# Kernel optimization log

Measured on AMD Instinct MI355X. Metric: run time of the kernel, lower is better.

## Reference

```python
import jax, jax.numpy as jnp
import numpy as np

NCAPS, NHIDDEN, NLAYER, ROUTIT = 8, 16, 2, 6
CUT = 5


def _normalize(v, axis):
    return v / jnp.maximum(jnp.linalg.norm(v, axis=axis, keepdims=True), 1e-12)


def _routing(x, nb_flat, k, max_iter, last):
    # x: [n, d] flat features, nb_flat: [n*m] neighbor ids (-1 = pad)
    n, d = x.shape
    dd = d // k
    m = nb_flat.shape[0] // n
    x3 = _normalize(x.reshape(n, k, dd), axis=2)              # [n,k,dd]
    x_c = jnp.concatenate([x3.reshape(n, d), jnp.zeros((1, d), x.dtype)], 0)  # [n+1,d]
    nbm = jnp.where(nb_flat < 0, n, nb_flat)
    z = x_c[nbm].reshape(n, m, k, dd)                         # neighbor gather
    u = None
    p = None
    for it in range(max_iter):
        p = jnp.zeros((n, m, k), x.dtype) if u is None else jnp.einsum('nmkc,nkc->nmk', z, u)
        p = jax.nn.softmax(p, axis=2)
        u = jnp.einsum('nmkc,nmk->nkc', z, p) + x3
        if it < max_iter - 1:
            u = _normalize(u, axis=2)
    if not last:
        return u.reshape(n, d)
    # meta-path aggregation (last layer)
    nb2 = nb_flat.reshape(n, m)
    nei_mask = (nb2 >= 0).astype(x.dtype)
    p1 = jnp.argmax(p, axis=2)                                # [n,m]
    A = jax.nn.one_hot(p1, k, dtype=x.dtype) * nei_mask[:, :, None]  # [n,m,k]
    Ai = A.transpose(2, 0, 1).astype(jnp.int32)               # [k,n,m]
    B = Ai * nb2[None].astype(jnp.int32) + (Ai - 1)           # nb where assigned, else -1
    B = jnp.concatenate([B, -jnp.ones((k, 1, m), jnp.int32)], axis=1)  # [k,n+1,m]
    mapB = jnp.where(B < 0, n, B)                             # -1 -> zero row n
    sel = mapB[:, :, :CUT]                                    # [k,n+1,CUT]
    x_c3 = x_c.reshape(n + 1, k, dd)
    gather_j = jax.vmap(lambda idx, xj: xj[idx], in_axes=(0, 1))  # over capsule j
    metas = []
    for i in range(k):
        # two-hop neighbors through capsule i then capsule j
        tmp = mapB[:, sel[i].reshape(-1), :CUT].reshape(k, n + 1, CUT * CUT)[:, :n]  # [k,n,25]
        hj = gather_j(tmp, x_c3)                               # [k,n,25,dd]
        metas.append(hj.mean(axis=2))                          # [k,n,dd]
    meta = jnp.stack(metas, 0)                                 # [i,j,n,dd]
    meta = meta.sum(axis=1).transpose(1, 0, 2)                 # sum over j -> [n,k,dd]
    meta = u + meta
    return u.reshape(n, d), meta.reshape(n, d)


def setup_inputs() -> dict:
    key = jax.random.key(0)
    ks = jax.random.split(key, 10)
    n, nfeat, nclass = 20000, 500, 16
    m = 32
    d = NCAPS * NHIDDEN
    return {
        'x': jax.random.normal(ks[0], (n, nfeat), jnp.float32),
        'nb': jax.random.randint(ks[1], (n, m), 0, n, jnp.int64),
        'pca_w': jax.random.normal(ks[2], (nfeat, d), jnp.float32) * 0.05,
        'pca_b': jax.random.normal(ks[3], (d,), jnp.float32) * 0.05,
        'ln_g': jnp.ones((NHIDDEN,), jnp.float32),
        'ln_b': jnp.zeros((NHIDDEN,), jnp.float32),
        'w_qs': jax.random.normal(ks[4], (NHIDDEN, NHIDDEN), jnp.float32) * 0.1,
        'w_ks': jax.random.normal(ks[5], (NHIDDEN, NHIDDEN), jnp.float32) * 0.1,
        'mlp_w': jax.random.normal(ks[6], (d, nclass), jnp.float32) * 0.05,
        'mlp_b': jax.random.normal(ks[7], (nclass,), jnp.float32) * 0.05,
    }


def reference(x, nb, pca_w, pca_b, ln_g, ln_b, w_qs, w_ks, mlp_w, mlp_b):
    k, dd = NCAPS, NHIDDEN
    n = x.shape[0]
    nb_flat = nb.reshape(-1)
    h = x @ pca_w + pca_b                                      # [n, d]
    h3 = h.reshape(n, k, dd)
    # Independence attention over capsules (only attn matters; output q is discarded)
    mu = h3.mean(-1, keepdims=True)
    var = ((h3 - mu) ** 2).mean(-1, keepdims=True)
    q = (h3 - mu) / jnp.sqrt(var + 1e-6) * ln_g + ln_b
    q = q @ w_qs                                               # [n,k,dd]
    kk = h3 @ w_ks
    temp = jnp.asarray(dd, x.dtype) ** 0.5
    attn = jax.nn.softmax(jnp.einsum('nqc,nkc->nqk', q / temp, kk), axis=-1)  # [n,k,k]
    off = 1.0 - jnp.eye(k, dtype=x.dtype)
    attn_loss = (attn * off).sum() / (off.sum() * n)
    h = jax.nn.relu(h3).reshape(n, k * dd)
    meta = None
    for layer in range(NLAYER):
        last = layer == NLAYER - 1
        if last:
            u, meta = _routing(h, nb_flat, k, ROUTIT, True)
        else:
            h = jax.nn.relu(_routing(h, nb_flat, k, ROUTIT, False))
    meta = jax.nn.relu(meta) @ mlp_w + mlp_b
    return jax.nn.log_softmax(meta, axis=1), attn_loss, meta
```

## Files before the change

kernel.cpp:

```cpp
#include <hip/hip_runtime.h>
#include <math.h>

#define NCAPS 8
#define DD    16
#define D     128
#define M     32
#define ROUTIT 6
#define CUT   5

__device__ __forceinline__ float wred16_sum(float v) {
    v += __shfl_xor(v, 1);
    v += __shfl_xor(v, 2);
    v += __shfl_xor(v, 4);
    v += __shfl_xor(v, 8);
    return v;
}

typedef _Float16 h2 __attribute__((ext_vector_type(2)));
union U32H2 { unsigned u; h2 h; };
__device__ __forceinline__ unsigned pack_h2(float a, float b) {
    U32H2 r; r.h.x = (_Float16)a; r.h.y = (_Float16)b; return r.u;
}
__device__ __forceinline__ h2 ash2(unsigned u) { U32H2 r; r.u = u; return r.h; }

__global__ void init_kernel(float* xc0, float* xc1, int n) {
    int t = threadIdx.x;
    if (t < D) {
        xc0[(size_t)n * D + t] = 0.f;
        xc1[(size_t)n * D + t] = 0.f;
    }
}

__global__ __launch_bounds__(256) void pca_attn(
        const float* __restrict__ x, const float* __restrict__ w,
        const float* __restrict__ bias, const float* __restrict__ ln_g,
        const float* __restrict__ ln_b, const float* __restrict__ w_qs,
        const float* __restrict__ w_ks, float* __restrict__ xc0,
        float* __restrict__ partial, int n, int nfeat) {
    __shared__ float xs[20][36];
    __shared__ alignas(16) float ws[20][128];
    __shared__ alignas(16) float hs[32][132];
    __shared__ alignas(16) float ks[32][8][20];
    __shared__ float wq[256], wk[256];
    __shared__ float red[4];
    const int tid = threadIdx.x;
    const int cg = tid & 31;
    const int rg = tid >> 5;
    const int row0 = blockIdx.x * 32;
    wq[tid] = w_qs[tid];
    wk[tid] = w_ks[tid];
    const float4 bi4 = *(const float4*)&bias[cg * 4];

    float acc[4][4] = {};
    for (int k0 = 0; k0 < nfeat; k0 += 20) {
        if (tid < 160) {
            int r = tid / 5, cf = tid % 5;
            int row = row0 + r;
            float4 f = (row < n)
                ? *(const float4*)&x[(size_t)row * nfeat + k0 + cf * 4]
                : make_float4(0.f, 0.f, 0.f, 0.f);
            xs[cf * 4 + 0][r] = f.x; xs[cf * 4 + 1][r] = f.y;
            xs[cf * 4 + 2][r] = f.z; xs[cf * 4 + 3][r] = f.w;
        }
#pragma unroll
        for (int i = 0; i < 3; ++i) {
            int f = tid + i * 256;
            if (f < 640) {
                int kk = f >> 5, c4 = f & 31;
                *(float4*)&ws[kk][c4 * 4] =
                    *(const float4*)&w[(size_t)(k0 + kk) * 128 + c4 * 4];
            }
        }
        __syncthreads();
#pragma unroll
        for (int kk = 0; kk < 20; ++kk) {
            float4 a = *(const float4*)&xs[kk][rg * 4];
            float4 b = *(const float4*)&ws[kk][cg * 4];
            float av[4] = {a.x, a.y, a.z, a.w};
            float bv[4] = {b.x, b.y, b.z, b.w};
#pragma unroll
            for (int i = 0; i < 4; ++i)
#pragma unroll
                for (int j = 0; j < 4; ++j) acc[i][j] += av[i] * bv[j];
        }
        __syncthreads();
    }
#pragma unroll
    for (int i = 0; i < 4; ++i)
        *(float4*)&hs[rg * 4 + i][cg * 4] =
            make_float4(acc[i][0] + bi4.x, acc[i][1] + bi4.y,
                        acc[i][2] + bi4.z, acc[i][3] + bi4.w);
    __syncthreads();

    const int r = tid >> 3, kq = tid & 7;
    const int row = row0 + r;
    float hv[16], q[16], kk[16];
    if (row < n) {
#pragma unroll
        for (int i = 0; i < 4; ++i) {
            float4 f = *(const float4*)&hs[r][kq * 16 + i * 4];
            hv[i * 4 + 0] = f.x; hv[i * 4 + 1] = f.y;
            hv[i * 4 + 2] = f.z; hv[i * 4 + 3] = f.w;
        }
        float mu = 0.f;
#pragma unroll
        for (int c = 0; c < 16; ++c) mu += hv[c];
        mu *= (1.f / 16.f);
        float var = 0.f;
#pragma unroll
        for (int c = 0; c < 16; ++c) { float d = hv[c] - mu; var += d * d; }
        var *= (1.f / 16.f);
        float rstd = rsqrtf(var + 1e-6f);
        float qn[16];
#pragma unroll
        for (int c = 0; c < 16; ++c)
            qn[c] = (hv[c] - mu) * rstd * ln_g[c] + ln_b[c];
#pragma unroll
        for (int c = 0; c < 16; ++c) { q[c] = 0.f; kk[c] = 0.f; }
#pragma unroll
        for (int cp = 0; cp < 16; ++cp)
#pragma unroll
            for (int c = 0; c < 16; ++c) {
                q[c]  += qn[cp] * wq[cp * 16 + c];
                kk[c] += hv[cp] * wk[cp * 16 + c];
            }
#pragma unroll
        for (int c = 0; c < 16; ++c) q[c] *= 0.25f;
#pragma unroll
        for (int i = 0; i < 4; ++i)
            *(float4*)&ks[r][kq][i * 4] =
                make_float4(kk[i * 4], kk[i * 4 + 1], kk[i * 4 + 2], kk[i * 4 + 3]);
        float ss = 0.f;
        float rl[16];
#pragma unroll
        for (int c = 0; c < 16; ++c) { rl[c] = fmaxf(hv[c], 0.f); ss += rl[c] * rl[c]; }
        float inv = 1.f / fmaxf(sqrtf(ss), 1e-12f);
        float4* xo = (float4*)(xc0 + (size_t)row * D + kq * DD);
#pragma unroll
        for (int i = 0; i < 4; ++i)
            xo[i] = make_float4(rl[i * 4] * inv, rl[i * 4 + 1] * inv,
                                rl[i * 4 + 2] * inv, rl[i * 4 + 3] * inv);
    }
    __syncthreads();

    float offd = 0.f;
    if (row < n) {
        float s[8];
#pragma unroll
        for (int j = 0; j < 8; ++j) {
            float d = 0.f;
#pragma unroll
            for (int i = 0; i < 4; ++i) {
                float4 f = *(const float4*)&ks[r][j][i * 4];
                d += q[i * 4] * f.x + q[i * 4 + 1] * f.y
                   + q[i * 4 + 2] * f.z + q[i * 4 + 3] * f.w;
            }
            s[j] = d;
        }
        float mx = s[0];
#pragma unroll
        for (int j = 1; j < 8; ++j) mx = fmaxf(mx, s[j]);
        float e[8], se = 0.f;
#pragma unroll
        for (int j = 0; j < 8; ++j) { e[j] = __expf(s[j] - mx); se += e[j]; }
        float rse = 1.f / se;
#pragma unroll
        for (int j = 0; j < 8; ++j)
            if (j != kq) offd += e[j] * rse;
    }
    offd += __shfl_xor(offd, 1);
    offd += __shfl_xor(offd, 2);
    offd += __shfl_xor(offd, 4);
    offd += __shfl_xor(offd, 8);
    offd += __shfl_xor(offd, 16);
    offd += __shfl_xor(offd, 32);
    int lane = tid & 63, wid = tid >> 6;
    if (lane == 0) red[wid] = offd;
    __syncthreads();
    if (tid == 0) partial[blockIdx.x] = red[0] + red[1] + red[2] + red[3];
}

__global__ __launch_bounds__(256) void reduce_kernel(
        const float* __restrict__ partial, float* __restrict__ acc, int npart) {
    __shared__ float red[4];
    const int t = threadIdx.x;
    float s = 0.f;
    for (int i = t; i < npart; i += 256) s += partial[i];
    s += __shfl_xor(s, 1);  s += __shfl_xor(s, 2);
    s += __shfl_xor(s, 4);  s += __shfl_xor(s, 8);
    s += __shfl_xor(s, 16); s += __shfl_xor(s, 32);
    if ((t & 63) == 0) red[t >> 6] = s;
    __syncthreads();
    if (t == 0) acc[0] = red[0] + red[1] + red[2] + red[3];
}

template <bool LAST>
__global__ __launch_bounds__(64) void routing_kernel(
        const float* __restrict__ xc,
        const int* __restrict__ nb,
        float* __restrict__ out,
        int* __restrict__ amax, int n) {
    __shared__ alignas(16) uint2 zsu[M * 32];
    __shared__ alignas(8)  uint2 usu[NCAPS * 5];
    __shared__ alignas(16) float pT[NCAPS * 36];
    const int l = threadIdx.x;
    const int v = blockIdx.x;
    const int m  = l & 31;
    const int kh = l >> 5;
    const int f4 = m;
    const int mg = kh;

    {
        int sm = l >> 1, sh = l & 1;
        int src = 0;
        if (l < M) {
            int nbv = nb[(size_t)v * M + l];
            src = (nbv < 0) ? n : nbv;
        }
        int srow = __shfl(src, sm);
        const float4* g = (const float4*)(xc + (size_t)srow * D);
#pragma unroll
        for (int i = 0; i < 16; ++i) {
            int f = sh * 16 + i;
            float4 zf = g[f];
            zsu[sm * 32 + (f ^ sm)] =
                make_uint2(pack_h2(zf.x, zf.y), pack_h2(zf.z, zf.w));
        }
    }
    float4 x3 = ((const float4*)(xc + (size_t)v * D))[f4];
    __syncthreads();

    {
        float4 a = make_float4(0.f, 0.f, 0.f, 0.f);
#pragma unroll
        for (int j = 0; j < 16; ++j) {
            int r = mg * 16 + j;
            uint2 zz = zsu[r * 32 + (f4 ^ r)];
            h2 lo = ash2(zz.x), hi = ash2(zz.y);
            a.x += (float)lo.x; a.y += (float)lo.y;
            a.z += (float)hi.x; a.w += (float)hi.y;
        }
        a.x += __shfl_xor(a.x, 32); a.y += __shfl_xor(a.y, 32);
        a.z += __shfl_xor(a.z, 32); a.w += __shfl_xor(a.w, 32);
        a.x = a.x * 0.125f + x3.x;  a.y = a.y * 0.125f + x3.y;
        a.z = a.z * 0.125f + x3.z;  a.w = a.w * 0.125f + x3.w;
        float ss = a.x * a.x + a.y * a.y + a.z * a.z + a.w * a.w;
        ss += __shfl_xor(ss, 1); ss += __shfl_xor(ss, 2);
        float inv = 1.f / fmaxf(sqrtf(ss), 1e-12f);
        if (l < 32)
            usu[(f4 >> 2) * 5 + (f4 & 3)] =
                make_uint2(pack_h2(a.x * inv, a.y * inv),
                           pack_h2(a.z * inv, a.w * inv));
    }
    __syncthreads();

    for (int it = 1; it < ROUTIT; ++it) {
        float pr[4];
#pragma unroll
        for (int j = 0; j < 4; ++j) {
            float s = 0.f;
            const uint2* uk = &usu[(kh * 4 + j) * 5];
#pragma unroll
            for (int c2 = 0; c2 < 4; ++c2) {
                int f = kh * 16 + j * 4 + c2;
                uint2 zz = zsu[m * 32 + (f ^ m)];
                uint2 uu = uk[c2];
                s = __builtin_amdgcn_fdot2(ash2(zz.x), ash2(uu.x), s, false);
                s = __builtin_amdgcn_fdot2(ash2(zz.y), ash2(uu.y), s, false);
            }
            pr[j] = s;
        }
        float po[4];
#pragma unroll
        for (int j = 0; j < 4; ++j) po[j] = __shfl_xor(pr[j], 32);
        if (LAST && it == ROUTIT - 1) {
            float p8[8];
#pragma unroll
            for (int j = 0; j < 4; ++j) {
                p8[kh * 4 + j] = pr[j];
                p8[(kh ^ 1) * 4 + j] = po[j];
            }
            float bv = p8[0]; int bi = 0;
#pragma unroll
            for (int k2 = 1; k2 < 8; ++k2)
                if (p8[k2] > bv) { bv = p8[k2]; bi = k2; }
            if (l < 32) amax[(size_t)v * M + m] = bi;
        }
        float er[4], S = 0.f;
#pragma unroll
        for (int j = 0; j < 4; ++j) { er[j] = __expf(pr[j]); S += er[j]; }
#pragma unroll
        for (int j = 0; j < 4; ++j) S += __expf(po[j]);
        float rS = 1.f / S;
#pragma unroll
        for (int j = 0; j < 4; ++j)
            pT[(kh * 4 + j) * 36 + m] = er[j] * rS;
        __syncthreads();

        float pk[16];
        {
            const int k2 = f4 >> 2;
#pragma unroll
            for (int j4 = 0; j4 < 4; ++j4) {
                float4 pp = *(const float4*)&pT[k2 * 36 + mg * 16 + j4 * 4];
                pk[j4 * 4 + 0] = pp.x; pk[j4 * 4 + 1] = pp.y;
                pk[j4 * 4 + 2] = pp.z; pk[j4 * 4 + 3] = pp.w;
            }
        }
        float4 a = make_float4(0.f, 0.f, 0.f, 0.f);
#pragma unroll
        for (int j = 0; j < 16; ++j) {
            int r = mg * 16 + j;
            uint2 zz = zsu[r * 32 + (f4 ^ r)];
            h2 lo = ash2(zz.x), hi = ash2(zz.y);
            a.x += (float)lo.x * pk[j]; a.y += (float)lo.y * pk[j];
            a.z += (float)hi.x * pk[j]; a.w += (float)hi.y * pk[j];
        }
        a.x += __shfl_xor(a.x, 32); a.y += __shfl_xor(a.y, 32);
        a.z += __shfl_xor(a.z, 32); a.w += __shfl_xor(a.w, 32);
        a.x += x3.x; a.y += x3.y; a.z += x3.z; a.w += x3.w;

        if (it < ROUTIT - 1) {
            float ss = a.x * a.x + a.y * a.y + a.z * a.z + a.w * a.w;
            ss += __shfl_xor(ss, 1); ss += __shfl_xor(ss, 2);
            float inv = 1.f / fmaxf(sqrtf(ss), 1e-12f);
            if (l < 32)
                usu[(f4 >> 2) * 5 + (f4 & 3)] =
                    make_uint2(pack_h2(a.x * inv, a.y * inv),
                               pack_h2(a.z * inv, a.w * inv));
            __syncthreads();
        } else if (LAST) {
            if (l < 32) ((float4*)(out + (size_t)v * D))[f4] = a;
        } else {
            float r0 = fmaxf(a.x, 0.f), r1 = fmaxf(a.y, 0.f);
            float r2 = fmaxf(a.z, 0.f), r3 = fmaxf(a.w, 0.f);
            float ss = r0 * r0 + r1 * r1 + r2 * r2 + r3 * r3;
            ss += __shfl_xor(ss, 1); ss += __shfl_xor(ss, 2);
            float inv = 1.f / fmaxf(sqrtf(ss), 1e-12f);
            if (l < 32)
                ((float4*)(out + (size_t)v * D))[f4] =
                    make_float4(r0 * inv, r1 * inv, r2 * inv, r3 * inv);
        }
    }
}

__global__ __launch_bounds__(256) void s2_kernel(
        const float* __restrict__ xc1, const int* __restrict__ nb,
        const int* __restrict__ amax, float* __restrict__ s2, int n) {
    int idx = blockIdx.x * 256 + threadIdx.x;
    if (idx >= n * 16) return;
    int w = idx >> 4, c = idx & 15;
    float s = 0.f;
#pragma unroll
    for (int b = 0; b < CUT; ++b) {
        int t  = nb[(size_t)w * M + b];
        int jj = amax[(size_t)w * M + b];
        int im = (t < 0) ? n : t;
        s += xc1[(size_t)im * D + jj * DD + c];
    }
    s2[idx] = s;
}

__global__ __launch_bounds__(256) void meta_kernel(
        const float* __restrict__ u1, const float* __restrict__ s2,
        const int* __restrict__ nb, const int* __restrict__ amax,
        const float* __restrict__ mlp_w, const float* __restrict__ mlp_b,
        const float* __restrict__ attn_acc, float* __restrict__ d_out, int n) {
    __shared__ float Wl[128 * 16];
    __shared__ float accs[16][132];
    const int t = threadIdx.x;
#pragma unroll
    for (int i = 0; i < 8; ++i) Wl[t + i * 256] = mlp_w[t + i * 256];
    const int g = t >> 4, c = t & 15;
    const int v = blockIdx.x * 16 + g;
    if (blockIdx.x == 0 && t == 0)
        d_out[(size_t)n * 16] = attn_acc[0] * (1.f / (56.f * (float)n));
    if (v < n) {
#pragma unroll
        for (int i = 0; i < 8; ++i) accs[g][i * 16 + c] = 0.f;
        for (int a = 0; a < CUT; ++a) {
            int w = nb[(size_t)v * M + a];
            if (w < 0) continue;
            int i = amax[(size_t)v * M + a];
            accs[g][i * 16 + c] += s2[(size_t)w * 16 + c];
        }
#pragma unroll
        for (int i = 0; i < 8; ++i) {
            float meta = u1[(size_t)v * D + i * 16 + c] + accs[g][i * 16 + c] * (1.f / 25.f);
            accs[g][i * 16 + c] = fmaxf(meta, 0.f);
        }
    }
    __syncthreads();
    if (v < n) {
        float o = mlp_b[c];
#pragma unroll
        for (int dd = 0; dd < 128; ++dd) o += accs[g][dd] * Wl[dd * 16 + c];
        float mx = o;
        mx = fmaxf(mx, __shfl_xor(mx, 1));
        mx = fmaxf(mx, __shfl_xor(mx, 2));
        mx = fmaxf(mx, __shfl_xor(mx, 4));
        mx = fmaxf(mx, __shfl_xor(mx, 8));
        float e = __expf(o - mx);
        float se = wred16_sum(e);
        float ls = (o - mx) - logf(se);
        d_out[(size_t)v * 16 + c] = ls;
        d_out[(size_t)n * 16 + 1 + (size_t)v * 16 + c] = o;
    }
}

extern "C" void kernel_launch(void* const* d_in, const int* in_sizes, int n_in,
                              void* d_out, int out_size, void* d_ws, size_t ws_size,
                              hipStream_t stream) {
    const float* x     = (const float*)d_in[0];
    const int*   nb    = (const int*)d_in[1];
    const float* pca_w = (const float*)d_in[2];
    const float* pca_b = (const float*)d_in[3];
    const float* ln_g  = (const float*)d_in[4];
    const float* ln_b  = (const float*)d_in[5];
    const float* w_qs  = (const float*)d_in[6];
    const float* w_ks  = (const float*)d_in[7];
    const float* mlp_w = (const float*)d_in[8];
    const float* mlp_b = (const float*)d_in[9];
    float* out = (float*)d_out;

    const int d = 128;
    const int nfeat = in_sizes[2] / d;
    const int n = in_sizes[0] / nfeat;
    const int nblk = (n + 31) / 32;

    float* bufA = (float*)d_ws;
    float* bufB = bufA + (size_t)n * d;
    float* bufC = bufB + (size_t)(n + 1) * d;
    float* acc  = bufC + (size_t)(n + 1) * d;
    int* amax = (int*)bufB;
    float* s2 = bufB + (size_t)n * M;
    float* partial = bufC;

    init_kernel<<<1, 256, 0, stream>>>(bufB, bufC, n);
    pca_attn<<<nblk, 256, 0, stream>>>(x, pca_w, pca_b, ln_g, ln_b, w_qs, w_ks,
                                       bufB, partial, n, nfeat);
    reduce_kernel<<<1, 256, 0, stream>>>(partial, acc, nblk);
    routing_kernel<false><<<n, 64, 0, stream>>>(bufB, nb, bufC, nullptr, n);
    routing_kernel<true><<<n, 64, 0, stream>>>(bufC, nb, bufA, amax, n);
    s2_kernel<<<(n * 16 + 255) / 256, 256, 0, stream>>>(bufC, nb, amax, s2, n);
    meta_kernel<<<(n + 15) / 16, 256, 0, stream>>>(bufA, s2, nb, amax, mlp_w, mlp_b, acc, out, n);
}
```

Measured before the change: 286.6 us.

## Use fp16 packed dot2 and register prefetch in PCA matmul

The PCA projection GEMM now converts input and weight tiles to packed fp16 pairs in shared memory and accumulates with v_dot2 (fdot2) in fp32. The next tile's global loads are prefetched into registers during the current tile's compute, so one barrier per tile is removed. Shared buffers are aliased to save LDS. This trades input precision (fp16 rounding of x and W) for fewer FMAs and less LDS traffic, which adds some accuracy risk.

```diff
diff --git a/kernel.cpp b/kernel.cpp
--- a/kernel.cpp
+++ b/kernel.cpp
@@ -37,10 +37,11 @@
         const float* __restrict__ ln_b, const float* __restrict__ w_qs,
         const float* __restrict__ w_ks, float* __restrict__ xc0,
         float* __restrict__ partial, int n, int nfeat) {
-    __shared__ float xs[20][36];
-    __shared__ alignas(16) float ws[20][128];
+    __shared__ alignas(16) unsigned char uS[20480];
+    unsigned (*xs2)[36]  = (unsigned(*)[36])uS;
+    unsigned (*ws2)[128] = (unsigned(*)[128])(uS + 1440);
+    float (*ks)[8][20]   = (float(*)[8][20])uS;
     __shared__ alignas(16) float hs[32][132];
-    __shared__ alignas(16) float ks[32][8][20];
     __shared__ float wq[256], wk[256];
     __shared__ float red[4];
     const int tid = threadIdx.x;
@@ -51,39 +52,75 @@
     wk[tid] = w_ks[tid];
     const float4 bi4 = *(const float4*)&bias[cg * 4];
 
+    const int xr_r = tid / 5, xr_cf = tid % 5;
+    const int wk0 = tid >> 5, wc0 = tid & 31;
+    float4 xr{}, w0a{}, w0b{}, w1a{}, w1b{};
+
+    {
+        if (tid < 160) {
+            int row = row0 + xr_r;
+            xr = (row < n) ? *(const float4*)&x[(size_t)row * nfeat + xr_cf * 4]
+                           : make_float4(0.f, 0.f, 0.f, 0.f);
+        }
+        w0a = *(const float4*)&w[(size_t)(2 * wk0) * 128 + wc0 * 4];
+        w0b = *(const float4*)&w[(size_t)(2 * wk0 + 1) * 128 + wc0 * 4];
+        if (tid < 64) {
+            int kkp = 8 + (tid >> 5);
+            w1a = *(const float4*)&w[(size_t)(2 * kkp) * 128 + wc0 * 4];
+            w1b = *(const float4*)&w[(size_t)(2 * kkp + 1) * 128 + wc0 * 4];
+        }
+    }
     float acc[4][4] = {};
-    for (int k0 = 0; k0 < nfeat; k0 += 20) {
+    const int ntile = nfeat / 20;
+    for (int t = 0; t < ntile; ++t) {
+        __syncthreads();
         if (tid < 160) {
-            int r = tid / 5, cf = tid % 5;
-            int row = row0 + r;
-            float4 f = (row < n)
-                ? *(const float4*)&x[(size_t)row * nfeat + k0 + cf * 4]
-                : make_float4(0.f, 0.f, 0.f, 0.f);
-            xs[cf * 4 + 0][r] = f.x; xs[cf * 4 + 1][r] = f.y;
-            xs[cf * 4 + 2][r] = f.z; xs[cf * 4 + 3][r] = f.w;
-        }
-#pragma unroll
-        for (int i = 0; i < 3; ++i) {
-            int f = tid + i * 256;
-            if (f < 640) {
-                int kk = f >> 5, c4 = f & 31;
-                *(float4*)&ws[kk][c4 * 4] =
-                    *(const float4*)&w[(size_t)(k0 + kk) * 128 + c4 * 4];
+            xs2[xr_cf * 2 + 0][xr_r] = pack_h2(xr.x, xr.y);
+            xs2[xr_cf * 2 + 1][xr_r] = pack_h2(xr.z, xr.w);
+        }
+        {
+            uint4 pw;
+            pw.x = pack_h2(w0a.x, w0b.x); pw.y = pack_h2(w0a.y, w0b.y);
+            pw.z = pack_h2(w0a.z, w0b.z); pw.w = pack_h2(w0a.w, w0b.w);
+            *(uint4*)&ws2[wk0][wc0 * 4] = pw;
+        }
+        if (tid < 64) {
+            int kkp = 8 + (tid >> 5);
+            uint4 pw;
+            pw.x = pack_h2(w1a.x, w1b.x); pw.y = pack_h2(w1a.y, w1b.y);
+            pw.z = pack_h2(w1a.z, w1b.z); pw.w = pack_h2(w1a.w, w1b.w);
+            *(uint4*)&ws2[kkp][wc0 * 4] = pw;
+        }
+        if (t < ntile - 1) {
+            int k0 = (t + 1) * 20;
+            if (tid < 160) {
+                int row = row0 + xr_r;
+                xr = (row < n)
+                    ? *(const float4*)&x[(size_t)row * nfeat + k0 + xr_cf * 4]
+                    : make_float4(0.f, 0.f, 0.f, 0.f);
+            }
+            w0a = *(const float4*)&w[(size_t)(k0 + 2 * wk0) * 128 + wc0 * 4];
+            w0b = *(const float4*)&w[(size_t)(k0 + 2 * wk0 + 1) * 128 + wc0 * 4];
+            if (tid < 64) {
+                int kkp = 8 + (tid >> 5);
+                w1a = *(const float4*)&w[(size_t)(k0 + 2 * kkp) * 128 + wc0 * 4];
+                w1b = *(const float4*)&w[(size_t)(k0 + 2 * kkp + 1) * 128 + wc0 * 4];
             }
         }
         __syncthreads();
 #pragma unroll
-        for (int kk = 0; kk < 20; ++kk) {
-            float4 a = *(const float4*)&xs[kk][rg * 4];
-            float4 b = *(const float4*)&ws[kk][cg * 4];
-            float av[4] = {a.x, a.y, a.z, a.w};
-            float bv[4] = {b.x, b.y, b.z, b.w};
+        for (int kkp = 0; kkp < 10; ++kkp) {
+            uint4 av = *(const uint4*)&xs2[kkp][rg * 4];
+            uint4 bv = *(const uint4*)&ws2[kkp][cg * 4];
+            unsigned aa[4] = {av.x, av.y, av.z, av.w};
+            unsigned bb[4] = {bv.x, bv.y, bv.z, bv.w};
 #pragma unroll
             for (int i = 0; i < 4; ++i)
 #pragma unroll
-                for (int j = 0; j < 4; ++j) acc[i][j] += av[i] * bv[j];
-        }
-        __syncthreads();
+                for (int j = 0; j < 4; ++j)
+                    acc[i][j] = __builtin_amdgcn_fdot2(ash2(aa[i]), ash2(bb[j]),
+                                                       acc[i][j], false);
+        }
     }
 #pragma unroll
     for (int i = 0; i < 4; ++i)
```

New measurement: 275.2 us. -4.0%, faster.
